# Kernel optimization log

Measured on AMD Instinct MI355X. Metric: run time of the kernel, lower is better.

## Reference

```python
import jax, jax.numpy as jnp
import numpy as np

# TrafficXLSTM defaults + xlstm-library internal defaults
D = 128          # embedding_dim
INNER = 256      # mLSTM proj_factor=2 -> inner dim
NH = 4           # mLSTM heads
DHM = INNER // NH
NB = INNER // 4  # qkv_proj_blocksize=4 -> block-diagonal 4x4 blocks
SNH = 4          # sLSTM heads
SDH = D // SNH
FF = 192         # gated FFN up dim: 1.3*128 rounded up to multiple of 64
K = 4            # causal conv kernel size
EPS = 1e-6
BLOCK_TYPES = ['m', 's', 'm', 's', 'm', 'm']  # slstm_at=[1,3], num_blocks=6
B, S, IN_SIZE, OUT_SIZE = 64, 256, 3, 3


def _ln(x, w):  # LayerNorm, weight only (xlstm default bias=False)
    mu = x.mean(-1, keepdims=True)
    var = x.var(-1, keepdims=True)
    return (x - mu) * jax.lax.rsqrt(var + EPS) * w


def _mh_norm(x, w):  # MultiHeadLayerNorm: per-head groupnorm. x: (B,S,NH,dh), w: (NH*dh,)
    mu = x.mean(-1, keepdims=True)
    var = x.var(-1, keepdims=True)
    xn = (x - mu) * jax.lax.rsqrt(var + EPS)
    b, s = x.shape[:2]
    return xn.reshape(b, s, -1) * w


def _causal_conv(x, w, b):  # depthwise causal conv1d. x: (B,S,C), w: (C,K), b: (C,)
    s = x.shape[1]
    xp = jnp.pad(x, ((0, 0), (K - 1, 0), (0, 0)))
    out = b
    for k in range(K):  # fixed small kernel
        out = out + xp[:, k:k + s, :] * w[:, k]
    return out


def _headwise(x, w):  # block-diagonal linear (LinearHeadwiseExpand). x: (B,S,INNER), w: (NB,4,4)
    b, s, _ = x.shape
    xb = x.reshape(b, s, NB, 4)
    return jnp.einsum('bsnk,nkl->bsnl', xb, w).reshape(b, s, -1)


def _mlstm_layer(x, Wup, cw, cb, Wq, Wk, Wv, Wig, big, Wfg, bfg, gnw, skip, Wdown):
    b, s, _ = x.shape
    up = x @ Wup                          # (B,S,2*INNER)
    x_m, z = up[..., :INNER], up[..., INNER:]
    xc = jax.nn.silu(_causal_conv(x_m, cw, cb))
    q = _headwise(xc, Wq)
    k = _headwise(xc, Wk)
    v = _headwise(x_m, Wv)
    qkv = jnp.concatenate([q, k, v], -1)  # gates read concat(q,k,v)
    ig = (qkv @ Wig + big).transpose(0, 2, 1)  # (B,NH,S)
    fg = (qkv @ Wfg + bfg).transpose(0, 2, 1)
    qh = q.reshape(b, s, NH, DHM).transpose(0, 2, 1, 3)  # (B,NH,S,dh)
    kh = k.reshape(b, s, NH, DHM).transpose(0, 2, 1, 3)
    vh = v.reshape(b, s, NH, DHM).transpose(0, 2, 1, 3)
    # parallel stabilized mLSTM (matrix-memory, vanilla backend math)
    logf = jax.nn.log_sigmoid(fg)
    cs = jnp.cumsum(logf, -1)
    logfg = cs[..., :, None] - cs[..., None, :]          # sum_{t=j+1..i} log f_t
    mask = jnp.tril(jnp.ones((s, s), bool))
    logD = jnp.where(mask, logfg + ig[..., None, :], -1e30)
    maxD = logD.max(-1, keepdims=True)
    Dm = jnp.exp(logD - maxD)
    scores = jnp.einsum('bhid,bhjd->bhij', qh, kh) * (DHM ** -0.5)
    C = scores * Dm
    n = jnp.maximum(jnp.abs(C.sum(-1, keepdims=True)), jnp.exp(-maxD)) + EPS
    h = jnp.einsum('bhij,bhjd->bhid', C / n, vh)         # (B,NH,S,dh)
    h = h.transpose(0, 2, 1, 3)                          # (B,S,NH,dh)
    hn = _mh_norm(h, gnw)
    out = (hn + skip * xc) * jax.nn.silu(z)              # learnable skip + output gate
    return out @ Wdown


def _slstm_layer(x, cw, cb, Wg, bg, R, gnw):
    b, s, _ = x.shape
    xc = jax.nn.silu(_causal_conv(x, cw, cb))

    def gate_in(inp, w, bias):  # block-diagonal headwise gate projection
        xb = inp.reshape(b, s, SNH, SDH)
        return jnp.einsum('bsnk,nkl->bsnl', xb, w) + bias.reshape(SNH, SDH)

    gi = gate_in(xc, Wg[0], bg[0])  # i,f gates read conv output
    gf = gate_in(xc, Wg[1], bg[1])
    gz = gate_in(x, Wg[2], bg[2])   # z,o gates read raw input
    go = gate_in(x, Wg[3], bg[3])
    gates = jnp.stack([gi, gf, gz, go], 0)       # (4,B,S,NH,dh)
    gates = jnp.moveaxis(gates, 2, 0)            # (S,4,B,NH,dh)

    def step(carry, g):
        c, n, h, m = carry                       # each (B,NH,dh)
        rec = jnp.einsum('bnk,gnkl->gbnl', h, R)  # block-diag recurrent contribution
        ir, fr = g[0] + rec[0], g[1] + rec[1]
        zr, orr = g[2] + rec[2], g[3] + rec[3]
        mnew = jnp.maximum(fr + m, ir)           # stabilizer state
        i = jnp.exp(ir - mnew)
        f = jnp.exp(fr + m - mnew)
        zt = jnp.tanh(zr)
        o = jax.nn.sigmoid(orr)
        cn = f * c + i * zt
        nn = f * n + i
        hn = o * cn / (nn + 1e-8)
        return (cn, nn, hn, mnew), hn

    z0 = jnp.zeros((b, SNH, SDH), x.dtype)
    _, ys = jax.lax.scan(step, (z0, z0, z0, z0), gates)
    ys = jnp.moveaxis(ys, 0, 1)                  # (B,S,NH,dh)
    return _mh_norm(ys, gnw)


def _ffn(x, Wup, Wdown):  # gated FFN of the sLSTM block
    u = x @ Wup
    g, v = u[..., :FF], u[..., FF:]
    return (jax.nn.gelu(g) * v) @ Wdown


def _forward(x, W_emb, b_emb, m_ln_w, m_Wup, m_conv_w, m_conv_b, m_Wq, m_Wk, m_Wv,
             m_Wig, m_big, m_Wfg, m_bfg, m_gn_w, m_skip, m_Wdown,
             s_ln_w, s_conv_w, s_conv_b, s_Wg, s_bg, s_R, s_gn_w, s_ln2_w,
             s_Wff_up, s_Wff_down, post_ln_w, W_out, b_out):
    h = x @ W_emb + b_emb  # input embedding (dropout = identity in eval)
    mi = si = 0
    for bt in BLOCK_TYPES:
        if bt == 'm':  # mLSTM block: x + mlstm(LN(x))
            h = h + _mlstm_layer(_ln(h, m_ln_w[mi]), m_Wup[mi], m_conv_w[mi], m_conv_b[mi],
                                 m_Wq[mi], m_Wk[mi], m_Wv[mi], m_Wig[mi], m_big[mi],
                                 m_Wfg[mi], m_bfg[mi], m_gn_w[mi], m_skip[mi], m_Wdown[mi])
            mi += 1
        else:          # sLSTM block: x + slstm(LN(x)); x + ffn(LN(x))
            h = h + _slstm_layer(_ln(h, s_ln_w[si]), s_conv_w[si], s_conv_b[si],
                                 s_Wg[si], s_bg[si], s_R[si], s_gn_w[si])
            h = h + _ffn(_ln(h, s_ln2_w[si]), s_Wff_up[si], s_Wff_down[si])
            si += 1
    h = _ln(h, post_ln_w)
    out = h[:, -1, :] @ W_out + b_out
    return out[:, None, :]  # (B, prediction_length=1, output_size)


def setup_inputs() -> dict:
    key = jax.random.key(0)
    ks = iter(jax.random.split(key, 64))

    def w(shape, fan_in):
        return jax.random.normal(next(ks), shape, jnp.float32) / np.sqrt(fan_in)

    nm, ns = 4, 2  # number of mLSTM / sLSTM blocks
    s_bg = jnp.zeros((ns, 4, D)).at[:, 1, :].set(3.0)  # positive forget-gate bias init
    return {
        'x': jax.random.normal(next(ks), (B, S, IN_SIZE), jnp.float32),
        'W_emb': w((IN_SIZE, D), IN_SIZE), 'b_emb': jnp.zeros((D,)),
        'm_ln_w': jnp.ones((nm, D)),
        'm_Wup': w((nm, D, 2 * INNER), D),
        'm_conv_w': w((nm, INNER, K), K), 'm_conv_b': jnp.zeros((nm, INNER)),
        'm_Wq': w((nm, NB, 4, 4), 4), 'm_Wk': w((nm, NB, 4, 4), 4), 'm_Wv': w((nm, NB, 4, 4), 4),
        'm_Wig': w((nm, 3 * INNER, NH), 3 * INNER), 'm_big': jnp.zeros((nm, NH)),
        'm_Wfg': w((nm, 3 * INNER, NH), 3 * INNER),
        'm_bfg': jnp.tile(jnp.linspace(3.0, 6.0, NH), (nm, 1)),
        'm_gn_w': jnp.ones((nm, INNER)), 'm_skip': jnp.ones((nm, INNER)),
        'm_Wdown': w((nm, INNER, D), INNER),
        's_ln_w': jnp.ones((ns, D)),
        's_conv_w': w((ns, D, K), K), 's_conv_b': jnp.zeros((ns, D)),
        's_Wg': w((ns, 4, SNH, SDH, SDH), SDH), 's_bg': s_bg,
        's_R': w((ns, 4, SNH, SDH, SDH), SDH),
        's_gn_w': jnp.ones((ns, D)), 's_ln2_w': jnp.ones((ns, D)),
        's_Wff_up': w((ns, D, 2 * FF), D), 's_Wff_down': w((ns, FF, D), FF),
        'post_ln_w': jnp.ones((D,)),
        'W_out': w((D, OUT_SIZE), D), 'b_out': jnp.zeros((OUT_SIZE,)),
    }


def reference(x, W_emb, b_emb, m_ln_w, m_Wup, m_conv_w, m_conv_b, m_Wq, m_Wk, m_Wv,
              m_Wig, m_big, m_Wfg, m_bfg, m_gn_w, m_skip, m_Wdown,
              s_ln_w, s_conv_w, s_conv_b, s_Wg, s_bg, s_R, s_gn_w, s_ln2_w,
              s_Wff_up, s_Wff_down, post_ln_w, W_out, b_out):
    return _forward(x, W_emb, b_emb, m_ln_w, m_Wup, m_conv_w, m_conv_b, m_Wq, m_Wk, m_Wv,
                    m_Wig, m_big, m_Wfg, m_bfg, m_gn_w, m_skip, m_Wdown,
                    s_ln_w, s_conv_w, s_conv_b, s_Wg, s_bg, s_R, s_gn_w, s_ln2_w,
                    s_Wff_up, s_Wff_down, post_ln_w, W_out, b_out)
```

## Files before the change

kernel.cpp:

```cpp
#include <hip/hip_runtime.h>
#include <hip/hip_bf16.h>

#define D_MODEL 128
#define INNER 256
#define NH 4
#define DHM 64
#define SNH 4
#define SDH 32
#define FF 192
#define CK 4
#define BATCH 64
#define SEQ 256
#define T_TOK (BATCH*SEQ)

typedef __hip_bfloat16 bf16;

__device__ __forceinline__ float sigf(float x){ return 1.0f/(1.0f+__expf(-x)); }
__device__ __forceinline__ float bcast_lane(float v, int k){
    return __uint_as_float(__builtin_amdgcn_readlane(__float_as_uint(v), k));
}
__device__ __forceinline__ float frcp(float x){ return __builtin_amdgcn_rcpf(x); }

__global__ void sentinel_kernel(float* __restrict__ out, float v)
{
    int idx = threadIdx.x;
    if (idx < BATCH*3) out[idx] = v;
}

__global__ void embed_kernel(const float* __restrict__ x, const float* __restrict__ W,
                             const float* __restrict__ bias, float* __restrict__ h)
{
    int idx = blockIdx.x*blockDim.x + threadIdx.x;
    if (idx >= T_TOK*D_MODEL) return;
    int d = idx & 127; int t = idx >> 7;
    float s = bias[d];
    #pragma unroll
    for (int i = 0; i < 3; ++i) s += x[t*3+i] * W[i*D_MODEL+d];
    h[idx] = s;
}

__global__ void ln_kernel(const float* __restrict__ x, const float* __restrict__ w,
                          float* __restrict__ out)
{
    int t = blockIdx.x; int lane = threadIdx.x;
    float v0 = x[(size_t)t*128 + lane], v1 = x[(size_t)t*128 + 64 + lane];
    float s = v0 + v1, ss = v0*v0 + v1*v1;
    #pragma unroll
    for (int off = 32; off >= 1; off >>= 1){ s += __shfl_xor(s,off); ss += __shfl_xor(ss,off); }
    float mu  = s * (1.f/128.f);
    float var = fmaxf(ss * (1.f/128.f) - mu*mu, 0.f);
    float r   = rsqrtf(var + 1e-6f);
    out[(size_t)t*128 + lane]      = (v0-mu)*r*w[lane];
    out[(size_t)t*128 + 64 + lane] = (v1-mu)*r*w[64+lane];
}

#define TM 64
#define TN 64
#define TK 32
__global__ void __launch_bounds__(256)
gemm_tiled_kernel(const float* __restrict__ A, const float* __restrict__ W,
                  float* __restrict__ C, int M, int N, int Kd, int acc)
{
    int ntiles = N / TN;
    int bx = blockIdx.x % ntiles;
    int by = blockIdx.x / ntiles;
    __shared__ float As[TK][TM+1];
    __shared__ float Ws[TK][TN];
    int tid = threadIdx.x;
    int tn = (tid & 15) * 4;
    int tm = (tid >> 4) * 4;
    float accr[4][4] = {{0.f}};
    for (int k0 = 0; k0 < Kd; k0 += TK){
        #pragma unroll
        for (int i = tid; i < TM*TK; i += 256){
            int c2 = i & 31, r = i >> 5;
            As[c2][r] = A[(size_t)(by*TM + r)*Kd + k0 + c2];
        }
        #pragma unroll
        for (int i = tid; i < TK*TN; i += 256){
            int c2 = i & 63, r = i >> 6;
            Ws[r][c2] = W[(size_t)(k0 + r)*N + bx*TN + c2];
        }
        __syncthreads();
        #pragma unroll
        for (int k = 0; k < TK; ++k){
            float a0 = As[k][tm], a1 = As[k][tm+1], a2 = As[k][tm+2], a3 = As[k][tm+3];
            float4 wv = *(const float4*)&Ws[k][tn];
            accr[0][0] = fmaf(a0, wv.x, accr[0][0]); accr[0][1] = fmaf(a0, wv.y, accr[0][1]);
            accr[0][2] = fmaf(a0, wv.z, accr[0][2]); accr[0][3] = fmaf(a0, wv.w, accr[0][3]);
            accr[1][0] = fmaf(a1, wv.x, accr[1][0]); accr[1][1] = fmaf(a1, wv.y, accr[1][1]);
            accr[1][2] = fmaf(a1, wv.z, accr[1][2]); accr[1][3] = fmaf(a1, wv.w, accr[1][3]);
            accr[2][0] = fmaf(a2, wv.x, accr[2][0]); accr[2][1] = fmaf(a2, wv.y, accr[2][1]);
            accr[2][2] = fmaf(a2, wv.z, accr[2][2]); accr[2][3] = fmaf(a2, wv.w, accr[2][3]);
            accr[3][0] = fmaf(a3, wv.x, accr[3][0]); accr[3][1] = fmaf(a3, wv.y, accr[3][1]);
            accr[3][2] = fmaf(a3, wv.z, accr[3][2]); accr[3][3] = fmaf(a3, wv.w, accr[3][3]);
        }
        __syncthreads();
    }
    #pragma unroll
    for (int i = 0; i < 4; ++i){
        size_t off = (size_t)(by*TM + tm + i)*N + bx*TN + tn;
        if (acc){
            float4 old = *(float4*)&C[off];
            old.x += accr[i][0]; old.y += accr[i][1];
            old.z += accr[i][2]; old.w += accr[i][3];
            *(float4*)&C[off] = old;
        } else {
            *(float4*)&C[off] = make_float4(accr[i][0], accr[i][1], accr[i][2], accr[i][3]);
        }
    }
}

__global__ void conv_silu_kernel(const float* __restrict__ in, int istride,
                                 const float* __restrict__ w, const float* __restrict__ bias,
                                 float* __restrict__ out, int C)
{
    int idx = blockIdx.x*blockDim.x + threadIdx.x;
    if (idx >= T_TOK*C) return;
    int c = idx % C; int t = idx / C;
    int s = t & (SEQ-1); int b = t >> 8;
    float a = bias[c];
    int j0 = (s >= CK-1) ? s-(CK-1) : 0;
    for (int j = j0; j <= s; ++j){
        int k = j - s + (CK-1);
        a += in[(size_t)(b*SEQ+j)*istride + c] * w[c*CK + k];
    }
    out[idx] = a * sigf(a);
}

__global__ void headwise_qk_kernel(const float* __restrict__ xc,
                                   const float* __restrict__ Wq, const float* __restrict__ Wk,
                                   float* __restrict__ qout, float* __restrict__ kout)
{
    int idx = blockIdx.x*blockDim.x + threadIdx.x;
    if (idx >= T_TOK*INNER) return;
    int c = idx & 255; int t = idx >> 8;
    int n = c >> 2, l = c & 3;
    const float* xr = xc + (size_t)t*256 + n*4;
    float x0 = xr[0], x1 = xr[1], x2 = xr[2], x3 = xr[3];
    const float* wq = Wq + n*16 + l;
    const float* wk = Wk + n*16 + l;
    qout[idx] = x0*wq[0] + x1*wq[4] + x2*wq[8] + x3*wq[12];
    kout[idx] = x0*wk[0] + x1*wk[4] + x2*wk[8] + x3*wk[12];
}

__global__ void headwise_inplace_kernel(float* __restrict__ up, const float* __restrict__ W)
{
    int idx = blockIdx.x*blockDim.x + threadIdx.x;
    if (idx >= T_TOK*64) return;
    int n = idx & 63; int t = idx >> 6;
    float* xr = up + (size_t)t*512 + n*4;
    float x0 = xr[0], x1 = xr[1], x2 = xr[2], x3 = xr[3];
    const float* w = W + n*16;
    for (int l = 0; l < 4; ++l)
        xr[l] = x0*w[l] + x1*w[4+l] + x2*w[8+l] + x3*w[12+l];
}

__global__ void __launch_bounds__(256)
gateproj_kernel(const float* __restrict__ q, const float* __restrict__ k,
                const float* __restrict__ up,
                const float* __restrict__ Wig, const float* __restrict__ big,
                const float* __restrict__ Wfg, const float* __restrict__ bfg,
                float* __restrict__ igt, float* __restrict__ fgt)
{
    int t = blockIdx.x*4 + (threadIdx.x >> 6);
    int lane = threadIdx.x & 63;
    float4 si = make_float4(0.f,0.f,0.f,0.f);
    float4 sf = make_float4(0.f,0.f,0.f,0.f);
    #pragma unroll
    for (int c = 0; c < 12; ++c){
        int j = c*64 + lane;
        float xv;
        if (c < 4)      xv = q[(size_t)t*256 + j];
        else if (c < 8) xv = k[(size_t)t*256 + j - 256];
        else            xv = up[(size_t)t*512 + j - 512];
        float4 wi = *(const float4*)(Wig + (size_t)j*4);
        float4 wf = *(const float4*)(Wfg + (size_t)j*4);
        si.x = fmaf(xv, wi.x, si.x); si.y = fmaf(xv, wi.y, si.y);
        si.z = fmaf(xv, wi.z, si.z); si.w = fmaf(xv, wi.w, si.w);
        sf.x = fmaf(xv, wf.x, sf.x); sf.y = fmaf(xv, wf.y, sf.y);
        sf.z = fmaf(xv, wf.z, sf.z); sf.w = fmaf(xv, wf.w, sf.w);
    }
    #pragma unroll
    for (int off = 32; off >= 1; off >>= 1){
        si.x += __shfl_xor(si.x, off); si.y += __shfl_xor(si.y, off);
        si.z += __shfl_xor(si.z, off); si.w += __shfl_xor(si.w, off);
        sf.x += __shfl_xor(sf.x, off); sf.y += __shfl_xor(sf.y, off);
        sf.z += __shfl_xor(sf.z, off); sf.w += __shfl_xor(sf.w, off);
    }
    int b = t >> 8, s = t & 255;
    int hh = lane & 3;
    float vi = (hh==0) ? si.x : (hh==1) ? si.y : (hh==2) ? si.z : si.w;
    float vf = (hh==0) ? sf.x : (hh==1) ? sf.y : (hh==2) ? sf.z : sf.w;
    if (lane < 4)       igt[(b*4+hh)*SEQ + s] = vi + big[hh];
    else if (lane < 8)  fgt[(b*4+hh)*SEQ + s] = vf + bfg[hh];
}

__global__ void __launch_bounds__(64)
cs_kernel(const float* __restrict__ fgt, const float* __restrict__ igt,
          float* __restrict__ cs, float* __restrict__ pm)
{
    int bh = blockIdx.x;
    int lane = threadIdx.x;
    float4 f4 = *(const float4*)(fgt + (size_t)bh*SEQ + lane*4);
    float4 i4 = *(const float4*)(igt + (size_t)bh*SEQ + lane*4);
    float lf0, lf1, lf2, lf3;
    { float f = f4.x; lf0 = (f > 0.f) ? -log1pf(__expf(-f)) : f - log1pf(__expf(f)); }
    { float f = f4.y; lf1 = (f > 0.f) ? -log1pf(__expf(-f)) : f - log1pf(__expf(f)); }
    { float f = f4.z; lf2 = (f > 0.f) ? -log1pf(__expf(-f)) : f - log1pf(__expf(f)); }
    { float f = f4.w; lf3 = (f > 0.f) ? -log1pf(__expf(-f)) : f - log1pf(__expf(f)); }
    float p0 = lf0, p1 = p0 + lf1, p2 = p1 + lf2, p3 = p2 + lf3;
    float incl = p3;
    #pragma unroll
    for (int off = 1; off < 64; off <<= 1){
        float v = __shfl_up(incl, off);
        if (lane >= off) incl += v;
    }
    float excl = __shfl_up(incl, 1);
    if (lane == 0) excl = 0.f;
    float c0 = excl + p0, c1 = excl + p1, c2 = excl + p2, c3 = excl + p3;
    *(float4*)(cs + (size_t)bh*SEQ + lane*4) = make_float4(c0, c1, c2, c3);
    float u0 = i4.x - c0, u1 = i4.y - c1, u2 = i4.z - c2, u3 = i4.w - c3;
    float m0 = u0, m1 = fmaxf(m0, u1), m2 = fmaxf(m1, u2), m3 = fmaxf(m2, u3);
    float inm = m3;
    #pragma unroll
    for (int off = 1; off < 64; off <<= 1){
        float v = __shfl_up(inm, off);
        if (lane >= off) inm = fmaxf(inm, v);
    }
    float exm = __shfl_up(inm, 1);
    if (lane == 0) exm = -1e30f;
    *(float4*)(pm + (size_t)bh*SEQ + lane*4) =
        make_float4(fmaxf(exm, m0), fmaxf(exm, m1), fmaxf(exm, m2), fmaxf(exm, m3));
}

#define AC 32
#define QB 64
__global__ void __launch_bounds__(256)
attn_kernel(float* __restrict__ q, const float* __restrict__ kk,
            const float* __restrict__ up,
            const float* __restrict__ igt, const float* __restrict__ cs,
            const float* __restrict__ pm)
{
    __shared__ float k_sh[AC][DHM];
    __shared__ float v_sh[AC][DHM];
    __shared__ float S_sh[QB][33];
    __shared__ float u_sh[SEQ];
    int blk = blockIdx.x;
    int bh = blk >> 2, qt = blk & 3;
    int b = bh >> 2, hh = bh & 3;
    int tid = threadIdx.x;
    int il = tid & 63;
    int g = tid >> 6;
    int i = qt*QB + il;
    u_sh[tid] = igt[bh*SEQ + tid] - cs[bh*SEQ + tid];
    float csi = cs[bh*SEQ + i];
    float m   = csi + pm[bh*SEQ + i];
    const float4* qp4 = (const float4*)(q + ((size_t)(b*SEQ + i)*INNER + hh*DHM));
    float4 qr4[16];
    #pragma unroll
    for (int r = 0; r < 16; ++r) qr4[r] = qp4[r];
    float4 acc4[4];
    #pragma unroll
    for (int r = 0; r < 4; ++r) acc4[r] = make_float4(0.f,0.f,0.f,0.f);
    float ssum = 0.f;
    int cend = (qt+1)*QB;

    for (int c0 = 0; c0 < cend; c0 += AC){
        {
            int half = tid >> 7;
            int idx2 = tid & 127;
            int r0 = idx2 >> 4;
            int d4 = idx2 & 15;
            #pragma unroll
            for (int rr = 0; rr < 4; ++rr){
                int r = r0 + rr*8;
                size_t tj = (size_t)(b*SEQ + c0 + r);
                if (half == 0)
                    ((float4*)&k_sh[r][0])[d4] = *(const float4*)(kk + tj*INNER + hh*DHM + d4*4);
                else
                    ((float4*)&v_sh[r][0])[d4] = *(const float4*)(up + tj*512 + hh*DHM + d4*4);
            }
        }
        __syncthreads();
        if (i >= c0){
            #pragma unroll
            for (int jj = 0; jj < 8; ++jj){
                int jl = g*8 + jj;
                const float4* kr = (const float4*)&k_sh[jl][0];
                float d0=0.f, d1=0.f, d2=0.f, d3=0.f;
                #pragma unroll
                for (int r4 = 0; r4 < 4; ++r4){
                    float4 ka = kr[r4*4+0], kb2 = kr[r4*4+1];
                    float4 kc = kr[r4*4+2], kd  = kr[r4*4+3];
                    float4 qa = qr4[r4*4+0], qb2 = qr4[r4*4+1];
                    float4 qc = qr4[r4*4+2], qd  = qr4[r4*4+3];
                    d0 += qa.x*ka.x + qa.y*ka.y + qa.z*ka.z + qa.w*ka.w;
                    d1 += qb2.x*kb2.x + qb2.y*kb2.y + qb2.z*kb2.z + qb2.w*kb2.w;
                    d2 += qc.x*kc.x + qc.y*kc.y + qc.z*kc.z + qc.w*kc.w;
                    d3 += qd.x*kd.x + qd.y*kd.y + qd.z*kd.z + qd.w*kd.w;
                }
                float dot = (d0+d1) + (d2+d3);
                int jg = c0 + jl;
                float arg = fminf(csi + u_sh[jg] - m, 0.f);
                S_sh[il][jl] = (jg <= i) ? dot * 0.125f * __expf(arg) : 0.f;
            }
        }
        __syncthreads();
        if (i >= c0){
            #pragma unroll
            for (int jj = 0; jj < AC; ++jj){
                float sv = S_sh[il][jj];
                ssum += sv;
                const float4* vr = (const float4*)&v_sh[jj][g*16];
                #pragma unroll
                for (int r = 0; r < 4; ++r){
                    float4 vv = vr[r];
                    acc4[r].x += sv*vv.x; acc4[r].y += sv*vv.y;
                    acc4[r].z += sv*vv.z; acc4[r].w += sv*vv.w;
                }
            }
        }
        __syncthreads();
    }
    float nrm = fmaxf(fabsf(ssum), __expf(-m)) + 1e-6f;
    float rn = 1.f/nrm;
    float4* op = (float4*)(q + ((size_t)(b*SEQ + i)*INNER + hh*DHM + g*16));
    #pragma unroll
    for (int r = 0; r < 4; ++r){
        float4 o = acc4[r];
        o.x *= rn; o.y *= rn; o.z *= rn; o.w *= rn;
        op[r] = o;
    }
}

__global__ void __launch_bounds__(256)
mh_gate_kernel(float* __restrict__ q, const float* __restrict__ up,
               const float* __restrict__ xc,
               const float* __restrict__ gnw, const float* __restrict__ skip)
{
    int unit = blockIdx.x*4 + (threadIdx.x >> 6);
    int lane = threadIdx.x & 63;
    int t = unit >> 2, hh = unit & 3;
    int c = hh*DHM + lane;
    float v = q[(size_t)t*256 + c];
    float s = v, ss = v*v;
    #pragma unroll
    for (int off = 32; off >= 1; off >>= 1){ s += __shfl_xor(s,off); ss += __shfl_xor(ss,off); }
    float mu  = s * (1.f/64.f);
    float var = fmaxf(ss * (1.f/64.f) - mu*mu, 0.f);
    float r   = rsqrtf(var + 1e-6f);
    float hn  = (v-mu)*r*gnw[c];
    float z   = up[(size_t)t*512 + 256 + c];
    q[(size_t)t*256 + c] = (hn + skip[c]*xc[(size_t)t*256 + c]) * (z*sigf(z));
}

#define SG_TOK 16
__global__ void __launch_bounds__(512)
slstm_gates_kernel(const float* __restrict__ xc, const float* __restrict__ xl,
                   const float* __restrict__ Wg, const float* __restrict__ bg,
                   float* __restrict__ gates)
{
    int tid = threadIdx.x;
    int l  = tid & 31;
    int gn = tid >> 5;
    int g  = gn >> 2, n = gn & 3;
    int t0 = blockIdx.x * SG_TOK;
    float wr[32];
    #pragma unroll
    for (int k = 0; k < 32; ++k) wr[k] = Wg[(size_t)gn*1024 + k*32 + l];
    float bias = bg[g*128 + n*32 + l];
    const float* xin = (g < 2) ? xc : xl;
    #pragma unroll 4
    for (int t = 0; t < SG_TOK; ++t){
        int tok = t0 + t;
        const float4* xr = (const float4*)(xin + (size_t)tok*128 + n*32);
        float a = bias;
        #pragma unroll
        for (int k4 = 0; k4 < 8; ++k4){
            float4 xv = xr[k4];
            a = fmaf(xv.x, wr[k4*4+0], a);
            a = fmaf(xv.y, wr[k4*4+1], a);
            a = fmaf(xv.z, wr[k4*4+2], a);
            a = fmaf(xv.w, wr[k4*4+3], a);
        }
        int b = tok >> 8, s = tok & 255;
        gates[(size_t)((b*4+n)*SEQ + s)*128 + l*4 + g] = a;
    }
}

__global__ void __launch_bounds__(64)
slstm_scan_kernel(const float* __restrict__ gates, const float* __restrict__ Rw,
                  float* __restrict__ ys)
{
    int bn = blockIdx.x;
    int b = bn >> 2, n = bn & 3;
    int lane = threadIdx.x;
    int l = lane & 31;
    int hi = lane >> 5;
    int gA = hi ? 2 : 0, gB = hi ? 3 : 1;
    const float* Rbase = Rw + (size_t)n*1024 + l;
    float Ra[32], Rb[32];
    #pragma unroll
    for (int k = 0; k < 32; ++k){
        Ra[k] = Rbase[(size_t)gA*4096 + k*32];
        Rb[k] = Rbase[(size_t)gB*4096 + k*32];
    }
    const float* gbase = gates + (size_t)bn*SEQ*128 + l*4 + (hi ? 2 : 0);
    float* yrow = ys + (size_t)b*SEQ*128 + n*32 + l;
    float2 g0 = *(const float2*)(gbase);
    float2 g1 = *(const float2*)(gbase + 128);
    float c = 0.f, nst = 0.f, m = 0.f, hst = 0.f;
    for (int s = 0; s < SEQ; ++s){
        float2 g2 = (s+2 < SEQ) ? *(const float2*)(gbase + (size_t)(s+2)*128)
                                : make_float2(0.f, 0.f);
        float ra0=0.f, ra1=0.f, ra2=0.f, ra3=0.f;
        float rb0=0.f, rb1=0.f, rb2=0.f, rb3=0.f;
        #pragma unroll
        for (int k = 0; k < 8; ++k){
            float h0 = bcast_lane(hst, k);
            float h1 = bcast_lane(hst, k+8);
            float h2 = bcast_lane(hst, k+16);
            float h3 = bcast_lane(hst, k+24);
            ra0 = fmaf(h0, Ra[k],    ra0); rb0 = fmaf(h0, Rb[k],    rb0);
            ra1 = fmaf(h1, Ra[k+8],  ra1); rb1 = fmaf(h1, Rb[k+8],  rb1);
            ra2 = fmaf(h2, Ra[k+16], ra2); rb2 = fmaf(h2, Rb[k+16], rb2);
            ra3 = fmaf(h3, Ra[k+24], ra3); rb3 = fmaf(h3, Rb[k+24], rb3);
        }
        float ra = (ra0+ra1) + (ra2+ra3);
        float rb = (rb0+rb1) + (rb2+rb3);
        float pa = g0.x + ra;
        float pb = g0.y + rb;
        float zr  = __shfl_xor(pa, 32);
        float orr = __shfl_xor(pb, 32);
        float mnew = fmaxf(pb + m, pa);
        float iv = __expf(pa - mnew);
        float fv = __expf(pb + m - mnew);
        float zt = 1.f - 2.f*frcp(1.f + __expf(2.f*zr));
        float ov = frcp(1.f + __expf(-orr));
        c   = fv*c + iv*zt;
        nst = fv*nst + iv;
        hst = ov * c * frcp(nst + 1e-8f);
        m = mnew;
        if (!hi) yrow[(size_t)s*128] = hst;
        g0 = g1; g1 = g2;
    }
}

__global__ void __launch_bounds__(256)
mh_add_kernel(const float* __restrict__ ys, const float* __restrict__ gnw,
              float* __restrict__ h)
{
    int unit = blockIdx.x*8 + (threadIdx.x >> 5);
    int l = threadIdx.x & 31;
    int t = unit >> 2, n = unit & 3;
    float v = ys[(size_t)t*128 + n*32 + l];
    float s = v, ss = v*v;
    #pragma unroll
    for (int off = 16; off >= 1; off >>= 1){ s += __shfl_xor(s,off); ss += __shfl_xor(ss,off); }
    float mu  = s * (1.f/32.f);
    float var = fmaxf(ss * (1.f/32.f) - mu*mu, 0.f);
    float r   = rsqrtf(var + 1e-6f);
    h[(size_t)t*128 + n*32 + l] += (v-mu)*r*gnw[n*32+l];
}

__global__ void geluv_kernel(const float* __restrict__ up, float* __restrict__ out)
{
    int idx = blockIdx.x*blockDim.x + threadIdx.x;
    if (idx >= T_TOK*FF) return;
    int j = idx % FF; int t = idx / FF;
    float g  = up[(size_t)t*384 + j];
    float vv = up[(size_t)t*384 + FF + j];
    float gel = 0.5f*g*(1.f + tanhf(0.7978845608028654f*(g + 0.044715f*g*g*g)));
    out[idx] = gel*vv;
}

__global__ void out_kernel(const float* __restrict__ ln, const float* __restrict__ W,
                           const float* __restrict__ bias, float* __restrict__ out)
{
    int idx = threadIdx.x;
    if (idx >= BATCH*3) return;
    int b = idx / 3, e = idx % 3;
    float s = bias[e];
    const float* xr = ln + ((size_t)(b*SEQ + SEQ-1))*128;
    for (int d = 0; d < 128; ++d) s += xr[d]*W[d*3+e];
    out[idx] = s;
}

#define LCHK do { \
    if (hipGetLastError() != hipSuccess){ \
        sentinel_kernel<<<1, 192, 0, stream>>>((float*)d_out, 3000.0f + 32.0f*(float)launch_idx); \
        return; } \
    ++launch_idx; } while(0)

extern "C" void kernel_launch(void* const* d_in, const int* in_sizes, int n_in,
                              void* d_out, int out_size, void* d_ws, size_t ws_size,
                              hipStream_t stream)
{
    (void)out_size;
    static const int expected_sizes[30] = {
        49152, 384, 128, 512, 262144, 4096, 1024, 4096, 4096, 4096,
        12288, 16, 12288, 16, 1024, 1024, 131072, 256, 1024, 256,
        32768, 1024, 32768, 256, 256, 98304, 49152, 128, 384, 3
    };
    if (n_in != 30){ sentinel_kernel<<<1,192,0,stream>>>((float*)d_out, 5000.0f); return; }
    for (int i = 0; i < 30; ++i)
        if (in_sizes[i] != expected_sizes[i]){
            sentinel_kernel<<<1,192,0,stream>>>((float*)d_out, 2000.0f + 32.0f*i); return; }
    if (ws_size < (size_t)96*1024*1024){
        sentinel_kernel<<<1,192,0,stream>>>((float*)d_out, 1000.0f + (float)(ws_size >> 20)); return; }

    const float* x        = (const float*)d_in[0];
    const float* W_emb    = (const float*)d_in[1];
    const float* b_emb    = (const float*)d_in[2];
    const float* m_ln_w   = (const float*)d_in[3];
    const float* m_Wup    = (const float*)d_in[4];
    const float* m_conv_w = (const float*)d_in[5];
    const float* m_conv_b = (const float*)d_in[6];
    const float* m_Wq     = (const float*)d_in[7];
    const float* m_Wk     = (const float*)d_in[8];
    const float* m_Wv     = (const float*)d_in[9];
    const float* m_Wig    = (const float*)d_in[10];
    const float* m_big    = (const float*)d_in[11];
    const float* m_Wfg    = (const float*)d_in[12];
    const float* m_bfg    = (const float*)d_in[13];
    const float* m_gn_w   = (const float*)d_in[14];
    const float* m_skip   = (const float*)d_in[15];
    const float* m_Wdown  = (const float*)d_in[16];
    const float* s_ln_w   = (const float*)d_in[17];
    const float* s_conv_w = (const float*)d_in[18];
    const float* s_conv_b = (const float*)d_in[19];
    const float* s_Wg     = (const float*)d_in[20];
    const float* s_bg     = (const float*)d_in[21];
    const float* s_R      = (const float*)d_in[22];
    const float* s_gn_w   = (const float*)d_in[23];
    const float* s_ln2_w  = (const float*)d_in[24];
    const float* s_Wff_up = (const float*)d_in[25];
    const float* s_Wff_dn = (const float*)d_in[26];
    const float* post_ln  = (const float*)d_in[27];
    const float* W_out    = (const float*)d_in[28];
    const float* b_out    = (const float*)d_in[29];

    float* ws  = (float*)d_ws;
    float* h   = ws;
    float* ln  = h   + (size_t)T_TOK*128;
    float* up  = ln  + (size_t)T_TOK*128;
    float* xc  = up  + (size_t)T_TOK*512;
    float* qb  = xc  + (size_t)T_TOK*256;
    float* kb  = qb  + (size_t)T_TOK*256;
    float* igt  = ln;
    float* fgt  = ln + 65536;
    float* csb  = ln + 2*65536;
    float* pmb  = ln + 3*65536;

    int launch_idx = 0;
    (void)hipGetLastError();

    embed_kernel<<<(T_TOK*128)/256, 256, 0, stream>>>(x, W_emb, b_emb, h); LCHK;

    const char* bt = "msmsmm";
    int mi = 0, si = 0;
    for (int blk = 0; blk < 6; ++blk){
        if (bt[blk] == 'm'){
            ln_kernel<<<T_TOK, 64, 0, stream>>>(h, m_ln_w + mi*128, ln); LCHK;
            gemm_tiled_kernel<<<(T_TOK/TM)*(512/TN), 256, 0, stream>>>(ln, m_Wup + (size_t)mi*65536, up, T_TOK, 512, 128, 0); LCHK;
            conv_silu_kernel<<<(T_TOK*256)/256, 256, 0, stream>>>(up, 512, m_conv_w + mi*1024, m_conv_b + mi*256, xc, 256); LCHK;
            headwise_qk_kernel<<<(T_TOK*256)/256, 256, 0, stream>>>(xc, m_Wq + mi*1024, m_Wk + mi*1024, qb, kb); LCHK;
            headwise_inplace_kernel<<<(T_TOK*64)/256, 256, 0, stream>>>(up, m_Wv + mi*1024); LCHK;
            gateproj_kernel<<<T_TOK/4, 256, 0, stream>>>(qb, kb, up, m_Wig + mi*3072, m_big + mi*4,
                                                         m_Wfg + mi*3072, m_bfg + mi*4, igt, fgt); LCHK;
            cs_kernel<<<BATCH*NH, 64, 0, stream>>>(fgt, igt, csb, pmb); LCHK;
            attn_kernel<<<BATCH*NH*4, 256, 0, stream>>>(qb, kb, up, igt, csb, pmb); LCHK;
            mh_gate_kernel<<<T_TOK, 256, 0, stream>>>(qb, up, xc, m_gn_w + mi*256, m_skip + mi*256); LCHK;
            gemm_tiled_kernel<<<(T_TOK/TM)*(128/TN), 256, 0, stream>>>(qb, m_Wdown + (size_t)mi*32768, h, T_TOK, 128, 256, 1); LCHK;
            ++mi;
        } else {
            ln_kernel<<<T_TOK, 64, 0, stream>>>(h, s_ln_w + si*128, ln); LCHK;
            conv_silu_kernel<<<(T_TOK*128)/256, 256, 0, stream>>>(ln, 128, s_conv_w + si*512, s_conv_b + si*128, xc, 128); LCHK;
            slstm_gates_kernel<<<T_TOK/SG_TOK, 512, 0, stream>>>(xc, ln, s_Wg + si*16384, s_bg + si*512, up); LCHK;
            slstm_scan_kernel<<<BATCH*4, 64, 0, stream>>>(up, s_R + si*16384, kb); LCHK;
            mh_add_kernel<<<T_TOK/2, 256, 0, stream>>>(kb, s_gn_w + si*128, h); LCHK;
            ln_kernel<<<T_TOK, 64, 0, stream>>>(h, s_ln2_w + si*128, ln); LCHK;
            gemm_tiled_kernel<<<(T_TOK/TM)*(384/TN), 256, 0, stream>>>(ln, s_Wff_up + (size_t)si*49152, up, T_TOK, 384, 128, 0); LCHK;
            geluv_kernel<<<(T_TOK*192)/256, 256, 0, stream>>>(up, qb); LCHK;
            gemm_tiled_kernel<<<(T_TOK/TM)*(128/TN), 256, 0, stream>>>(qb, s_Wff_dn + (size_t)si*24576, h, T_TOK, 128, 192, 1); LCHK;
            ++si;
        }
    }

    ln_kernel<<<T_TOK, 64, 0, stream>>>(h, post_ln, ln); LCHK;
    out_kernel<<<1, 192, 0, stream>>>(ln, W_out, b_out, (float*)d_out); LCHK;
}
```

Measured before the change: 1.701 ms.

## Add 128x64 GEMM tile for up-projections and pair causal attention query tiles

Adds a GEMM variant with a 128-row by 64-column tile and an 8x4 per-thread micro-tile, and uses it for the mLSTM up-projection and the FFN up-projection. The larger tile is meant to improve arithmetic intensity and cut shared-memory traffic. The attention kernel now runs each block over two query tiles, a long one (3-pair) and a short one (pair), which balances the causal triangular work and halves the grid. The trade-offs are more registers in the GEMM and fewer blocks in attention, which lowers occupancy and parallelism.

```diff
diff --git a/kernel.cpp b/kernel.cpp
--- a/kernel.cpp
+++ b/kernel.cpp
@@ -100,6 +100,64 @@
     #pragma unroll
     for (int i = 0; i < 4; ++i){
         size_t off = (size_t)(by*TM + tm + i)*N + bx*TN + tn;
+        if (acc){
+            float4 old = *(float4*)&C[off];
+            old.x += accr[i][0]; old.y += accr[i][1];
+            old.z += accr[i][2]; old.w += accr[i][3];
+            *(float4*)&C[off] = old;
+        } else {
+            *(float4*)&C[off] = make_float4(accr[i][0], accr[i][1], accr[i][2], accr[i][3]);
+        }
+    }
+}
+
+#define HM 128
+#define HN 64
+#define HK 32
+__global__ void __launch_bounds__(256)
+gemm_tiled_m128_kernel(const float* __restrict__ A, const float* __restrict__ W,
+                       float* __restrict__ C, int M, int N, int Kd, int acc)
+{
+    int ntiles = N / HN;
+    int bx = blockIdx.x % ntiles;
+    int by = blockIdx.x / ntiles;
+    __shared__ float As[HK][HM+4];
+    __shared__ float Ws[HK][HN];
+    int tid = threadIdx.x;
+    int tn = (tid & 15) * 4;
+    int tm = (tid >> 4) * 8;
+    float accr[8][4] = {{0.f}};
+    for (int k0 = 0; k0 < Kd; k0 += HK){
+        #pragma unroll
+        for (int i = tid; i < HM*HK; i += 256){
+            int c2 = i & 31, r = i >> 5;
+            As[c2][r] = A[(size_t)(by*HM + r)*Kd + k0 + c2];
+        }
+        #pragma unroll
+        for (int i = tid; i < HK*HN; i += 256){
+            int c2 = i & 63, r = i >> 6;
+            Ws[r][c2] = W[(size_t)(k0 + r)*N + bx*HN + c2];
+        }
+        __syncthreads();
+        #pragma unroll
+        for (int k = 0; k < HK; ++k){
+            float4 a0 = *(const float4*)&As[k][tm];
+            float4 a1 = *(const float4*)&As[k][tm+4];
+            float4 wv = *(const float4*)&Ws[k][tn];
+            float av[8] = {a0.x,a0.y,a0.z,a0.w,a1.x,a1.y,a1.z,a1.w};
+            #pragma unroll
+            for (int ii = 0; ii < 8; ++ii){
+                accr[ii][0] = fmaf(av[ii], wv.x, accr[ii][0]);
+                accr[ii][1] = fmaf(av[ii], wv.y, accr[ii][1]);
+                accr[ii][2] = fmaf(av[ii], wv.z, accr[ii][2]);
+                accr[ii][3] = fmaf(av[ii], wv.w, accr[ii][3]);
+            }
+        }
+        __syncthreads();
+    }
+    #pragma unroll
+    for (int i = 0; i < 8; ++i){
+        size_t off = (size_t)(by*HM + tm + i)*N + bx*HN + tn;
         if (acc){
             float4 old = *(float4*)&C[off];
             old.x += accr[i][0]; old.y += accr[i][1];
@@ -247,90 +305,94 @@
     __shared__ float S_sh[QB][33];
     __shared__ float u_sh[SEQ];
     int blk = blockIdx.x;
-    int bh = blk >> 2, qt = blk & 3;
+    int bh = blk >> 1, pair = blk & 1;
     int b = bh >> 2, hh = bh & 3;
     int tid = threadIdx.x;
     int il = tid & 63;
     int g = tid >> 6;
-    int i = qt*QB + il;
     u_sh[tid] = igt[bh*SEQ + tid] - cs[bh*SEQ + tid];
-    float csi = cs[bh*SEQ + i];
-    float m   = csi + pm[bh*SEQ + i];
-    const float4* qp4 = (const float4*)(q + ((size_t)(b*SEQ + i)*INNER + hh*DHM));
-    float4 qr4[16];
-    #pragma unroll
-    for (int r = 0; r < 16; ++r) qr4[r] = qp4[r];
-    float4 acc4[4];
-    #pragma unroll
-    for (int r = 0; r < 4; ++r) acc4[r] = make_float4(0.f,0.f,0.f,0.f);
-    float ssum = 0.f;
-    int cend = (qt+1)*QB;
-
-    for (int c0 = 0; c0 < cend; c0 += AC){
-        {
-            int half = tid >> 7;
-            int idx2 = tid & 127;
-            int r0 = idx2 >> 4;
-            int d4 = idx2 & 15;
-            #pragma unroll
-            for (int rr = 0; rr < 4; ++rr){
-                int r = r0 + rr*8;
-                size_t tj = (size_t)(b*SEQ + c0 + r);
-                if (half == 0)
-                    ((float4*)&k_sh[r][0])[d4] = *(const float4*)(kk + tj*INNER + hh*DHM + d4*4);
-                else
-                    ((float4*)&v_sh[r][0])[d4] = *(const float4*)(up + tj*512 + hh*DHM + d4*4);
-            }
-        }
-        __syncthreads();
-        if (i >= c0){
-            #pragma unroll
-            for (int jj = 0; jj < 8; ++jj){
-                int jl = g*8 + jj;
-                const float4* kr = (const float4*)&k_sh[jl][0];
-                float d0=0.f, d1=0.f, d2=0.f, d3=0.f;
+
+    for (int pass = 0; pass < 2; ++pass){
+        int qt = pass ? pair : (3 - pair);
+        int i = qt*QB + il;
+        float csi = cs[bh*SEQ + i];
+        float m   = csi + pm[bh*SEQ + i];
+        const float4* qp4 = (const float4*)(q + ((size_t)(b*SEQ + i)*INNER + hh*DHM));
+        float4 qr4[16];
+        #pragma unroll
+        for (int r = 0; r < 16; ++r) qr4[r] = qp4[r];
+        float4 acc4[4];
+        #pragma unroll
+        for (int r = 0; r < 4; ++r) acc4[r] = make_float4(0.f,0.f,0.f,0.f);
+        float ssum = 0.f;
+        int cend = (qt+1)*QB;
+
+        for (int c0 = 0; c0 < cend; c0 += AC){
+            {
+                int half = tid >> 7;
+                int idx2 = tid & 127;
+                int r0 = idx2 >> 4;
+                int d4 = idx2 & 15;
                 #pragma unroll
-                for (int r4 = 0; r4 < 4; ++r4){
-                    float4 ka = kr[r4*4+0], kb2 = kr[r4*4+1];
-                    float4 kc = kr[r4*4+2], kd  = kr[r4*4+3];
-                    float4 qa = qr4[r4*4+0], qb2 = qr4[r4*4+1];
-                    float4 qc = qr4[r4*4+2], qd  = qr4[r4*4+3];
-                    d0 += qa.x*ka.x + qa.y*ka.y + qa.z*ka.z + qa.w*ka.w;
-                    d1 += qb2.x*kb2.x + qb2.y*kb2.y + qb2.z*kb2.z + qb2.w*kb2.w;
-                    d2 += qc.x*kc.x + qc.y*kc.y + qc.z*kc.z + qc.w*kc.w;
-                    d3 += qd.x*kd.x + qd.y*kd.y + qd.z*kd.z + qd.w*kd.w;
-                }
-                float dot = (d0+d1) + (d2+d3);
-                int jg = c0 + jl;
-                float arg = fminf(csi + u_sh[jg] - m, 0.f);
-                S_sh[il][jl] = (jg <= i) ? dot * 0.125f * __expf(arg) : 0.f;
-            }
-        }
-        __syncthreads();
-        if (i >= c0){
-            #pragma unroll
-            for (int jj = 0; jj < AC; ++jj){
-                float sv = S_sh[il][jj];
-                ssum += sv;
-                const float4* vr = (const float4*)&v_sh[jj][g*16];
-                #pragma unroll
-                for (int r = 0; r < 4; ++r){
-                    float4 vv = vr[r];
-                    acc4[r].x += sv*vv.x; acc4[r].y += sv*vv.y;
-                    acc4[r].z += sv*vv.z; acc4[r].w += sv*vv.w;
+                for (int rr = 0; rr < 4; ++rr){
+                    int r = r0 + rr*8;
+                    size_t tj = (size_t)(b*SEQ + c0 + r);
+                    if (half == 0)
+                        ((float4*)&k_sh[r][0])[d4] = *(const float4*)(kk + tj*INNER + hh*DHM + d4*4);
+                    else
+                        ((float4*)&v_sh[r][0])[d4] = *(const float4*)(up + tj*512 + hh*DHM + d4*4);
                 }
             }
-        }
-        __syncthreads();
-    }
-    float nrm = fmaxf(fabsf(ssum), __expf(-m)) + 1e-6f;
-    float rn = 1.f/nrm;
-    float4* op = (float4*)(q + ((size_t)(b*SEQ + i)*INNER + hh*DHM + g*16));
-    #pragma unroll
-    for (int r = 0; r < 4; ++r){
-        float4 o = acc4[r];
-        o.x *= rn; o.y *= rn; o.z *= rn; o.w *= rn;
-        op[r] = o;
+            __syncthreads();
+            if (i >= c0){
+                #pragma unroll
+                for (int jj = 0; jj < 8; ++jj){
+                    int jl = g*8 + jj;
+                    const float4* kr = (const float4*)&k_sh[jl][0];
+                    float d0=0.f, d1=0.f, d2=0.f, d3=0.f;
+                    #pragma unroll
+                    for (int r4 = 0; r4 < 4; ++r4){
+                        float4 ka = kr[r4*4+0], kb2 = kr[r4*4+1];
+                        float4 kc = kr[r4*4+2], kd  = kr[r4*4+3];
+                        float4 qa = qr4[r4*4+0], qb2 = qr4[r4*4+1];
+                        float4 qc = qr4[r4*4+2], qd  = qr4[r4*4+3];
+                        d0 += qa.x*ka.x + qa.y*ka.y + qa.z*ka.z + qa.w*ka.w;
+                        d1 += qb2.x*kb2.x + qb2.y*kb2.y + qb2.z*kb2.z + qb2.w*kb2.w;
+                        d2 += qc.x*kc.x + qc.y*kc.y + qc.z*kc.z + qc.w*kc.w;
+                        d3 += qd.x*kd.x + qd.y*kd.y + qd.z*kd.z + qd.w*kd.w;
+                    }
+                    float dot = (d0+d1) + (d2+d3);
+                    int jg = c0 + jl;
+                    float arg = fminf(csi + u_sh[jg] - m, 0.f);
+                    S_sh[il][jl] = (jg <= i) ? dot * 0.125f * __expf(arg) : 0.f;
+                }
+            }
+            __syncthreads();
+            if (i >= c0){
+                #pragma unroll
+                for (int jj = 0; jj < AC; ++jj){
+                    float sv = S_sh[il][jj];
+                    ssum += sv;
+                    const float4* vr = (const float4*)&v_sh[jj][g*16];
+                    #pragma unroll
+                    for (int r = 0; r < 4; ++r){
+                        float4 vv = vr[r];
+                        acc4[r].x += sv*vv.x; acc4[r].y += sv*vv.y;
+                        acc4[r].z += sv*vv.z; acc4[r].w += sv*vv.w;
+                    }
+                }
+            }
+            __syncthreads();
+        }
+        float nrm = fmaxf(fabsf(ssum), __expf(-m)) + 1e-6f;
+        float rn = 1.f/nrm;
+        float4* op = (float4*)(q + ((size_t)(b*SEQ + i)*INNER + hh*DHM + g*16));
+        #pragma unroll
+        for (int r = 0; r < 4; ++r){
+            float4 o = acc4[r];
+            o.x *= rn; o.y *= rn; o.z *= rn; o.w *= rn;
+            op[r] = o;
+        }
     }
 }
 
@@ -563,14 +625,14 @@
     for (int blk = 0; blk < 6; ++blk){
         if (bt[blk] == 'm'){
             ln_kernel<<<T_TOK, 64, 0, stream>>>(h, m_ln_w + mi*128, ln); LCHK;
-            gemm_tiled_kernel<<<(T_TOK/TM)*(512/TN), 256, 0, stream>>>(ln, m_Wup + (size_t)mi*65536, up, T_TOK, 512, 128, 0); LCHK;
+            gemm_tiled_m128_kernel<<<(T_TOK/HM)*(512/HN), 256, 0, stream>>>(ln, m_Wup + (size_t)mi*65536, up, T_TOK, 512, 128, 0); LCHK;
             conv_silu_kernel<<<(T_TOK*256)/256, 256, 0, stream>>>(up, 512, m_conv_w + mi*1024, m_conv_b + mi*256, xc, 256); LCHK;
             headwise_qk_kernel<<<(T_TOK*256)/256, 256, 0, stream>>>(xc, m_Wq + mi*1024, m_Wk + mi*1024, qb, kb); LCHK;
             headwise_inplace_kernel<<<(T_TOK*64)/256, 256, 0, stream>>>(up, m_Wv + mi*1024); LCHK;
             gateproj_kernel<<<T_TOK/4, 256, 0, stream>>>(qb, kb, up, m_Wig + mi*3072, m_big + mi*4,
                                                          m_Wfg + mi*3072, m_bfg + mi*4, igt, fgt); LCHK;
             cs_kernel<<<BATCH*NH, 64, 0, stream>>>(fgt, igt, csb, pmb); LCHK;
-            attn_kernel<<<BATCH*NH*4, 256, 0, stream>>>(qb, kb, up, igt, csb, pmb); LCHK;
+            attn_kernel<<<BATCH*NH*2, 256, 0, stream>>>(qb, kb, up, igt, csb, pmb); LCHK;
             mh_gate_kernel<<<T_TOK, 256, 0, stream>>>(qb, up, xc, m_gn_w + mi*256, m_skip + mi*256); LCHK;
             gemm_tiled_kernel<<<(T_TOK/TM)*(128/TN), 256, 0, stream>>>(qb, m_Wdown + (size_t)mi*32768, h, T_TOK, 128, 256, 1); LCHK;
             ++mi;
@@ -581,7 +643,7 @@
             slstm_scan_kernel<<<BATCH*4, 64, 0, stream>>>(up, s_R + si*16384, kb); LCHK;
             mh_add_kernel<<<T_TOK/2, 256, 0, stream>>>(kb, s_gn_w + si*128, h); LCHK;
             ln_kernel<<<T_TOK, 64, 0, stream>>>(h, s_ln2_w + si*128, ln); LCHK;
-            gemm_tiled_kernel<<<(T_TOK/TM)*(384/TN), 256, 0, stream>>>(ln, s_Wff_up + (size_t)si*49152, up, T_TOK, 384, 128, 0); LCHK;
+            gemm_tiled_m128_kernel<<<(T_TOK/HM)*(384/HN), 256, 0, stream>>>(ln, s_Wff_up + (size_t)si*49152, up, T_TOK, 384, 128, 0); LCHK;
             geluv_kernel<<<(T_TOK*192)/256, 256, 0, stream>>>(up, qb); LCHK;
             gemm_tiled_kernel<<<(T_TOK/TM)*(128/TN), 256, 0, stream>>>(qb, s_Wff_dn + (size_t)si*24576, h, T_TOK, 128, 192, 1); LCHK;
             ++si;
```

Result: faster. 1.569 ms (-7.7%).
